# Optimization experiments

Measured on AMD Instinct MI355X. Metric: run time of the kernel, lower is better.

The kernel has to match this reference:

```python
import jax, jax.numpy as jnp
import numpy as np
import math

B, S, D, H = 2, 2048, 1024, 16
DK = D // H  # 64
THETA = 500000.0


def setup_inputs() -> dict:
    key = jax.random.key(0)
    ks = jax.random.split(key, 6)
    x = jax.random.normal(ks[0], (B, S, D), dtype=jnp.float32)
    # RoPE frequencies: inv_freq = theta^{-(2i/dk)}, angles = pos * inv_freq
    inv_freq = 1.0 / (THETA ** (jnp.arange(0, DK, 2, dtype=jnp.float32) / DK))  # [DK/2]
    angles = jnp.arange(S, dtype=jnp.float32)[:, None] * inv_freq[None, :]      # [S, DK/2]
    freqs_cos = jnp.cos(angles)
    freqs_sin = jnp.sin(angles)
    # causal additive mask [B, S, S]: 0 on/below diagonal, -1e9 above
    causal = jnp.tril(jnp.ones((S, S), dtype=bool))
    mask = jnp.where(causal, 0.0, -1e9).astype(jnp.float32)
    mask = jnp.broadcast_to(mask, (B, S, S))
    scale = 0.02
    wq = jax.random.normal(ks[1], (D, D), dtype=jnp.float32) * scale
    wk = jax.random.normal(ks[2], (D, D), dtype=jnp.float32) * scale
    wv = jax.random.normal(ks[3], (D, D), dtype=jnp.float32) * scale
    wo = jax.random.normal(ks[4], (D, D), dtype=jnp.float32) * scale
    return {"x": x, "freqs_cos": freqs_cos, "freqs_sin": freqs_sin,
            "mask": mask, "wq": wq, "wk": wk, "wv": wv, "wo": wo}


def _apply_rope(t, cos, sin):
    # t: [B, S, H, DK]; cos/sin: [S, DK/2]
    tr = t.reshape(*t.shape[:-1], DK // 2, 2)
    t0, t1 = tr[..., 0], tr[..., 1]
    c = cos[None, :, None, :]
    s = sin[None, :, None, :]
    out = jnp.stack([t0 * c - t1 * s, t0 * s + t1 * c], axis=-1)
    return out.reshape(*t.shape)


def reference(x, freqs_cos, freqs_sin, mask, wq, wk, wv, wo):
    b, s, d = x.shape
    # nn.Linear(bias=False): y = x @ W^T, W is [out, in]
    q = jnp.einsum('bsd,ed->bse', x, wq).reshape(b, s, H, DK)
    k = jnp.einsum('bsd,ed->bse', x, wk).reshape(b, s, H, DK)
    v = jnp.einsum('bsd,ed->bse', x, wv).reshape(b, s, H, DK)
    q = _apply_rope(q, freqs_cos, freqs_sin)
    k = _apply_rope(k, freqs_cos, freqs_sin)
    inv_sqrt_dk = 1.0 / math.sqrt(DK)
    # scores: [B, H, S, S]
    scores = jnp.einsum('bqhd,bkhd->bhqk', q, k) * inv_sqrt_dk
    scores = scores + mask[:, None, :, :]
    # NOTE: the original module divides by sqrt(d_k) a SECOND time before softmax
    attn = jax.nn.softmax(scores * inv_sqrt_dk, axis=-1)
    out = jnp.einsum('bhqk,bkhd->bqhd', attn, v).reshape(b, s, d)
    return jnp.einsum('bsd,ed->bse', out, wo)
```

## Files before the change

kernel.cpp:

```cpp
#include <hip/hip_runtime.h>
#include <stdint.h>

#define Bq 2
#define Sq 2048
#define Dq 1024
#define Hq 16
#define DKq 64

typedef unsigned short u16;
typedef __attribute__((ext_vector_type(8))) __bf16 bf8;
typedef __attribute__((ext_vector_type(4))) __bf16 bf4;
typedef __attribute__((ext_vector_type(4))) float fx4;
typedef __attribute__((ext_vector_type(8))) unsigned short us8;
typedef __attribute__((ext_vector_type(4))) unsigned short us4;

__device__ __forceinline__ u16 f2bf(float f) {
    union { float f; unsigned int i; } v; v.f = f;
    unsigned int r = v.i + 0x7FFFu + ((v.i >> 16) & 1u);
    return (u16)(r >> 16);
}

__device__ __forceinline__ void gll16(const void* g, void* l) {
    typedef __attribute__((address_space(1))) void GV;
    typedef __attribute__((address_space(3))) void LV;
    __builtin_amdgcn_global_load_lds((GV*)g, (LV*)l, 16, 0, 0);
}

template<int N> __device__ __forceinline__ void waitv() {
    asm volatile("s_waitcnt vmcnt(%0)" :: "n"(N) : "memory");
}

__global__ void __launch_bounds__(256) cvt_all(const float* __restrict__ x,
                                               const float* __restrict__ wq,
                                               const float* __restrict__ wk,
                                               const float* __restrict__ wv,
                                               const float* __restrict__ wo,
                                               u16* __restrict__ ws) {
    int blk = blockIdx.x;
    const float* s;
    u16* d;
    int i;
    if (blk < 4096)      { s = x;  d = ws;           i = blk * 256 + threadIdx.x; }
    else if (blk < 5120) { s = wq; d = ws + 4194304; i = (blk - 4096) * 256 + threadIdx.x; }
    else if (blk < 6144) { s = wk; d = ws + 5242880; i = (blk - 5120) * 256 + threadIdx.x; }
    else if (blk < 7168) { s = wv; d = ws + 6291456; i = (blk - 6144) * 256 + threadIdx.x; }
    else                 { s = wo; d = ws + 7340032; i = (blk - 7168) * 256 + threadIdx.x; }
    float4 v = *(const float4*)(s + (size_t)i * 4);
    us4 o;
    o[0] = f2bf(v.x); o[1] = f2bf(v.y); o[2] = f2bf(v.z); o[3] = f2bf(v.w);
    *(us4*)(d + (size_t)i * 4) = o;
}

template<int MODE>
__global__ void __launch_bounds__(512, 1) gemm_bt(
    const u16* __restrict__ A,
    const u16* __restrict__ W0, const u16* __restrict__ W1, const u16* __restrict__ W2,
    u16* __restrict__ O0, u16* __restrict__ O1, u16* __restrict__ O2,
    float* __restrict__ Of,
    const float* __restrict__ fc, const float* __restrict__ fs)
{
    constexpr int K = 1024;
    constexpr int NT = 32;
    __shared__ __align__(16) u16 As[3][256 * 32];
    __shared__ __align__(16) u16 Bs[3][256 * 32];
    const int tid = threadIdx.x;
    const int lane = tid & 63, wid = tid >> 6;
    const int wr = wid >> 2, wc = wid & 3;
    const int fr = lane & 15, fq = lane >> 4;

    int wgid = blockIdx.x;
    int Xc = wgid & 7, jj = wgid >> 3;
    int by, bx, bz;
    if (MODE == 1) {
        int T = Xc * 24 + jj;
        by = T / 12;
        int p = T - by * 12;
        bz = p >> 2; bx = p & 3;
    } else {
        int T = Xc * 8 + jj;
        by = T >> 2; bx = T & 3; bz = 0;
    }
    const int m0 = by * 256, n0 = bx * 256;

    const u16* Wm = W0;
    u16* Ob = O0;
    if (MODE == 1) {
        if (bz == 1)      { Wm = W1; Ob = O1; }
        else if (bz == 2) { Wm = W2; Ob = O2; }
    }

    const u16* ga = A  + (size_t)(m0 + (tid >> 2)) * K + (tid & 3) * 8;
    const u16* gb = Wm + (size_t)(n0 + (tid >> 2)) * K + (tid & 3) * 8;

    fx4 acc[8][4] = {};

    auto STAGE_A = [&](int t, int b) {
        gll16(ga + t * 32,           As[b] + tid * 8);
        gll16(ga + 128 * K + t * 32, As[b] + tid * 8 + 4096);
    };
    auto STAGE_B = [&](int t, int b) {
        gll16(gb + t * 32,           Bs[b] + tid * 8);
        gll16(gb + 128 * K + t * 32, Bs[b] + tid * 8 + 4096);
    };

    STAGE_A(0, 0); STAGE_B(0, 0);
    STAGE_A(1, 1); STAGE_B(1, 1);
    waitv<4>();
    __builtin_amdgcn_sched_barrier(0);
    __builtin_amdgcn_s_barrier();
    __builtin_amdgcn_sched_barrier(0);

    int b0 = 0;
    #pragma unroll 1
    for (int t = 0; t < NT; ++t) {
        const u16* Ab = As[b0];
        const u16* Bb = Bs[b0];
        const int bn = b0 + 2 >= 3 ? b0 - 1 : b0 + 2;
        bf8 bfr[4];
        #pragma unroll
        for (int nj = 0; nj < 4; ++nj)
            bfr[nj] = *(const bf8*)(&Bb[(wc * 64 + nj * 16 + fr) * 32 + fq * 8]);

        #pragma unroll
        for (int ph = 0; ph < 2; ++ph) {
            bf8 af[4];
            #pragma unroll
            for (int mi = 0; mi < 4; ++mi)
                af[mi] = *(const bf8*)(&Ab[(wr * 128 + ph * 64 + mi * 16 + fr) * 32 + fq * 8]);
            if (t + 2 < NT) {
                if (ph == 0) STAGE_A(t + 2, bn);
                else         STAGE_B(t + 2, bn);
            }
            __builtin_amdgcn_sched_barrier(0);
            __builtin_amdgcn_s_barrier();
            __builtin_amdgcn_sched_barrier(0);
            __builtin_amdgcn_s_setprio(1);
            #pragma unroll
            for (int mi = 0; mi < 4; ++mi)
                #pragma unroll
                for (int nj = 0; nj < 4; ++nj)
                    acc[ph * 4 + mi][nj] = __builtin_amdgcn_mfma_f32_16x16x32_bf16(
                        af[mi], bfr[nj], acc[ph * 4 + mi][nj], 0, 0, 0);
            __builtin_amdgcn_s_setprio(0);
            __builtin_amdgcn_sched_barrier(0);
            if (ph == 1) {
                if (t < NT - 2) waitv<4>();
                else            waitv<0>();
                __builtin_amdgcn_sched_barrier(0);
            }
            __builtin_amdgcn_s_barrier();
            __builtin_amdgcn_sched_barrier(0);
        }
        b0 = b0 + 1 >= 3 ? 0 : b0 + 1;
    }

    if (MODE == 0) {
        #pragma unroll
        for (int mi = 0; mi < 8; ++mi)
            #pragma unroll
            for (int nj = 0; nj < 4; ++nj)
                #pragma unroll
                for (int r = 0; r < 4; ++r) {
                    int m = m0 + wr * 128 + mi * 16 + fq * 4 + r;
                    int n = n0 + wc * 64 + nj * 16 + fr;
                    Of[(size_t)m * 1024 + n] = acc[mi][nj][r];
                }
    } else if (bz == 2) {
        #pragma unroll
        for (int mi = 0; mi < 8; ++mi)
            #pragma unroll
            for (int nj = 0; nj < 4; ++nj) {
                int n = n0 + wc * 64 + nj * 16 + fr;
                int mb = m0 + wr * 128 + mi * 16 + fq * 4;
                int b = mb >> 11, s = mb & 2047;
                int h = n >> 6, dk = n & 63;
                bf4 pk;
                #pragma unroll
                for (int r = 0; r < 4; ++r) pk[r] = (__bf16)acc[mi][nj][r];
                *(bf4*)((__bf16*)Ob + (((size_t)(b * Hq + h)) * DKq + dk) * Sq + s) = pk;
            }
    } else {
        #pragma unroll
        for (int mi = 0; mi < 8; ++mi)
            #pragma unroll
            for (int nj = 0; nj < 4; ++nj) {
                int n = n0 + wc * 64 + nj * 16 + fr;
                int h = n >> 6, dk = n & 63;
                int ip = dk >> 1;
                float sgn = (dk & 1) ? 1.f : -1.f;
                #pragma unroll
                for (int r = 0; r < 4; ++r) {
                    int m = m0 + wr * 128 + mi * 16 + fq * 4 + r;
                    int b = m >> 11, s = m & 2047;
                    float v = acc[mi][nj][r];
                    float pv = __shfl_xor(v, 1);
                    float c  = fc[s * 32 + ip];
                    float sn = fs[s * 32 + ip];
                    float o = v * c + sgn * pv * sn;
                    ((__bf16*)Ob)[(((size_t)(b * Hq + h)) * Sq + s) * DKq + dk] = (__bf16)o;
                }
            }
    }
}

__device__ __forceinline__ int swz(int row) { return ((row & 7) ^ ((row >> 3) & 7)) << 4; }

__global__ void __launch_bounds__(512, 4) attn_k(const u16* __restrict__ Q,
                                                 const u16* __restrict__ Kg,
                                                 const u16* __restrict__ Vtg,
                                                 u16* __restrict__ AO) {
    int L = blockIdx.x + 32 * blockIdx.y;
    int X = L & 7, C = L >> 3;
    const int bh = X * 4 + (C & 3);
    const int Qt = 31 - (C >> 2);
    const int b = bh >> 4, h = bh & 15;
    const int tid = threadIdx.x, lane = tid & 63, wid = tid >> 6;
    const int wq4 = wid & 3, par = wid >> 2;
    const int fr = lane & 15, fq = lane >> 4;
    const int swzfr = swz(fr);

    __shared__ __align__(16) u16 Ks[2][64 * 64];
    __shared__ __align__(16) u16 Vs[2][64 * 64];
    __shared__ __align__(16) u16 Ps[8][16 * 64];
    __shared__ float Lx[4][64];

    const u16* Kp = Kg  + (size_t)bh * Sq * 64;
    const u16* Vp = Vtg + (size_t)bh * 64 * Sq;
    const int q0 = Qt * 64;
    const int nt = Qt + 1;
    const int NS = (nt + 1) >> 1;

    bf8 qf0, qf1;
    {
        const u16* Qp = Q + ((size_t)bh * Sq + q0) * 64;
        int qr = wq4 * 16 + fr;
        qf0 = *(const bf8*)(Qp + qr * 64 + fq * 8);
        qf1 = *(const bf8*)(Qp + qr * 64 + fq * 8 + 32);
    }

    fx4 oacc[4] = {};
    float l_loc = 0.f;

    const int srow = tid >> 3;
    const int sce  = (tid & 7) * 8;
    const int ldst = srow * 128 + (((tid & 7) * 16) ^ swz(srow));

    us8 kreg[2], vreg[2];
    #pragma unroll
    for (int c = 0; c < 2; ++c) {
        int t = c < nt ? c : nt - 1;
        kreg[c] = *(const us8*)(Kp + ((size_t)t * 64 + srow) * 64 + sce);
        vreg[c] = *(const us8*)(Vp + (size_t)srow * Sq + t * 64 + sce);
    }
    #pragma unroll
    for (int c = 0; c < 2; ++c) {
        *(us8*)((char*)Ks[c] + ldst) = kreg[c];
        *(us8*)((char*)Vs[c] + ldst) = vreg[c];
    }
    if (NS > 1) {
        #pragma unroll
        for (int c = 0; c < 2; ++c) {
            int t = 2 + c < nt ? 2 + c : nt - 1;
            kreg[c] = *(const us8*)(Kp + ((size_t)t * 64 + srow) * 64 + sce);
            vreg[c] = *(const us8*)(Vp + (size_t)srow * Sq + t * 64 + sce);
        }
    }
    __syncthreads();

    #pragma unroll 1
    for (int sp = 0; sp < NS; ++sp) {
        const int t = 2 * sp + par;
        if (t < nt) {
            const char* Kb = (const char*)Ks[par];
            const char* Vb = (const char*)Vs[par];
            char* Pw = (char*)Ps[wid] + fr * 128;

            fx4 sf[4];
            __builtin_amdgcn_s_setprio(1);
            #pragma unroll
            for (int sj = 0; sj < 4; ++sj) {
                int krow = sj * 16 + fr;
                bf8 kf0 = *(const bf8*)(Kb + krow * 128 + ((fq * 16) ^ swz(krow)));
                bf8 kf1 = *(const bf8*)(Kb + krow * 128 + ((64 + fq * 16) ^ swz(krow)));
                fx4 a = {0.f, 0.f, 0.f, 0.f};
                a = __builtin_amdgcn_mfma_f32_16x16x32_bf16(kf0, qf0, a, 0, 0, 0);
                a = __builtin_amdgcn_mfma_f32_16x16x32_bf16(kf1, qf1, a, 0, 0, 0);
                sf[sj] = a;
            }
            __builtin_amdgcn_s_setprio(0);

            float pv[4][4];
            #pragma unroll
            for (int sj = 0; sj < 4; ++sj)
                #pragma unroll
                for (int r = 0; r < 4; ++r)
                    pv[sj][r] = __expf(sf[sj][r] * 0.015625f);
            if (t == Qt) {
                int ql = wq4 * 16 + fr;
                #pragma unroll
                for (int sj = 0; sj < 4; ++sj)
                    #pragma unroll
                    for (int r = 0; r < 4; ++r)
                        if (sj * 16 + fq * 4 + r > ql) pv[sj][r] = 0.f;
            }
            #pragma unroll
            for (int sj = 0; sj < 4; ++sj) {
                bf4 w;
                #pragma unroll
                for (int r = 0; r < 4; ++r) { w[r] = (__bf16)pv[sj][r]; l_loc += pv[sj][r]; }
                *(bf4*)(Pw + ((sj * 32 + fq * 8) ^ swzfr)) = w;
            }

            __builtin_amdgcn_s_setprio(1);
            #pragma unroll
            for (int kk = 0; kk < 2; ++kk) {
                bf8 pf = *(const bf8*)(Pw + ((kk * 64 + fq * 16) ^ swzfr));
                #pragma unroll
                for (int mf = 0; mf < 4; ++mf) {
                    int vrow = mf * 16 + fr;
                    bf8 vf = *(const bf8*)(Vb + vrow * 128 + ((kk * 64 + fq * 16) ^ swz(vrow)));
                    oacc[mf] = __builtin_amdgcn_mfma_f32_16x16x32_bf16(vf, pf, oacc[mf], 0, 0, 0);
                }
            }
            __builtin_amdgcn_s_setprio(0);
        }
        __syncthreads();
        if (sp + 1 < NS) {
            #pragma unroll
            for (int c = 0; c < 2; ++c) {
                *(us8*)((char*)Ks[c] + ldst) = kreg[c];
                *(us8*)((char*)Vs[c] + ldst) = vreg[c];
            }
            if (sp + 2 < NS) {
                #pragma unroll
                for (int c = 0; c < 2; ++c) {
                    int tt = 2 * (sp + 2) + c; if (tt > nt - 1) tt = nt - 1;
                    kreg[c] = *(const us8*)(Kp + ((size_t)tt * 64 + srow) * 64 + sce);
                    vreg[c] = *(const us8*)(Vp + (size_t)srow * Sq + tt * 64 + sce);
                }
            }
            __syncthreads();
        }
    }

    l_loc += __shfl_xor(l_loc, 16);
    l_loc += __shfl_xor(l_loc, 32);
    if (par == 1) {
        float* ob = (float*)Ps + wq4 * 1024;
        #pragma unroll
        for (int mf = 0; mf < 4; ++mf)
            *(fx4*)(ob + lane * 16 + mf * 4) = oacc[mf];
        Lx[wq4][lane] = l_loc;
    }
    __syncthreads();
    if (par == 0) {
        const float* ob = (float*)Ps + wq4 * 1024;
        float lt = l_loc + Lx[wq4][lane];
        float linv = __builtin_amdgcn_rcpf(lt);
        int s = q0 + wq4 * 16 + fr;
        #pragma unroll
        for (int mf = 0; mf < 4; ++mf) {
            fx4 oh = *(const fx4*)(ob + lane * 16 + mf * 4);
            bf4 pk;
            #pragma unroll
            for (int r = 0; r < 4; ++r) pk[r] = (__bf16)((oacc[mf][r] + oh[r]) * linv);
            *(bf4*)((__bf16*)AO + ((size_t)(b * Sq + s)) * Dq + h * 64 + mf * 16 + fq * 4) = pk;
        }
    }
}

extern "C" void kernel_launch(void* const* d_in, const int* in_sizes, int n_in,
                              void* d_out, int out_size, void* d_ws, size_t ws_size,
                              hipStream_t stream) {
    const float* x  = (const float*)d_in[0];
    const float* fc = (const float*)d_in[1];
    const float* fs = (const float*)d_in[2];
    const float* wq = (const float*)d_in[4];
    const float* wk = (const float*)d_in[5];
    const float* wv = (const float*)d_in[6];
    const float* wo = (const float*)d_in[7];
    float* out = (float*)d_out;

    u16* ws  = (u16*)d_ws;
    u16* xb  = ws;
    u16* wqb = ws + 4194304;
    u16* wkb = ws + 5242880;
    u16* wvb = ws + 6291456;
    u16* wob = ws + 7340032;
    u16* Qb  = ws + 8388608;
    u16* Kb  = ws + 12582912;
    u16* Vb  = ws + 16777216;
    u16* AOb = ws + 20971520;

    cvt_all<<<8192, 256, 0, stream>>>(x, wq, wk, wv, wo, ws);

    gemm_bt<1><<<192, 512, 0, stream>>>(xb, wqb, wkb, wvb, Qb, Kb, Vb, nullptr, fc, fs);

    dim3 g2(32, 32, 1);
    attn_k<<<g2, 512, 0, stream>>>(Qb, Kb, Vb, AOb);

    gemm_bt<0><<<64, 512, 0, stream>>>(AOb, wob, nullptr, nullptr, nullptr, nullptr, nullptr, out, nullptr, nullptr);
}
```

Measured before the change: 128.1 us.

## Shrink GEMM tiles to 128-row blocks, add LDS swizzle and deeper prefetch

The projection GEMMs move from 256x256 tiles to 128x256 (QKV) and 128x128 (output) tiles, raising block counts from 192/64 to 384/256 so more of the GPU's compute units are filled. Launch bounds now allow up to 4 blocks per SM. An XOR swizzle on the K-column chunk is added to cut LDS bank conflicts, and the pipeline is simplified to one phase per k-step with three stages prefetched up front. The trade-off is less data reuse per tile and more global traffic per FLOP.

```diff
diff --git a/kernel.cpp b/kernel.cpp
--- a/kernel.cpp
+++ b/kernel.cpp
@@ -29,6 +29,7 @@
 template<int N> __device__ __forceinline__ void waitv() {
     asm volatile("s_waitcnt vmcnt(%0)" :: "n"(N) : "memory");
 }
+__device__ __forceinline__ void SB() { __builtin_amdgcn_sched_barrier(0); }
 
 __global__ void __launch_bounds__(256) cvt_all(const float* __restrict__ x,
                                                const float* __restrict__ wq,
@@ -52,7 +53,7 @@
 }
 
 template<int MODE>
-__global__ void __launch_bounds__(512, 1) gemm_bt(
+__global__ void __launch_bounds__(512, 4) gemm_bt(
     const u16* __restrict__ A,
     const u16* __restrict__ W0, const u16* __restrict__ W1, const u16* __restrict__ W2,
     u16* __restrict__ O0, u16* __restrict__ O1, u16* __restrict__ O2,
@@ -61,8 +62,15 @@
 {
     constexpr int K = 1024;
     constexpr int NT = 32;
-    __shared__ __align__(16) u16 As[3][256 * 32];
-    __shared__ __align__(16) u16 Bs[3][256 * 32];
+    constexpr int BN = MODE ? 256 : 128;
+    constexpr int WN = BN / 4;
+    constexpr int NJ = WN / 16;
+    constexpr int BOPS = BN / 128;
+    constexpr int SOPS = 1 + BOPS;
+    constexpr int ASZ = 128 * 32;
+    constexpr int BSZ = BN * 32;
+    __shared__ __align__(16) u16 As[3 * ASZ];
+    __shared__ __align__(16) u16 Bs[3 * BSZ];
     const int tid = threadIdx.x;
     const int lane = tid & 63, wid = tid >> 6;
     const int wr = wid >> 2, wc = wid & 3;
@@ -72,15 +80,15 @@
     int Xc = wgid & 7, jj = wgid >> 3;
     int by, bx, bz;
     if (MODE == 1) {
-        int T = Xc * 24 + jj;
+        int T = Xc * 48 + jj;
         by = T / 12;
         int p = T - by * 12;
         bz = p >> 2; bx = p & 3;
     } else {
-        int T = Xc * 8 + jj;
-        by = T >> 2; bx = T & 3; bz = 0;
-    }
-    const int m0 = by * 256, n0 = bx * 256;
+        int T = Xc * 32 + jj;
+        by = T >> 3; bx = T & 7; bz = 0;
+    }
+    const int m0 = by * 128, n0 = bx * BN;
 
     const u16* Wm = W0;
     u16* Ob = O0;
@@ -89,89 +97,69 @@
         else if (bz == 2) { Wm = W2; Ob = O2; }
     }
 
-    const u16* ga = A  + (size_t)(m0 + (tid >> 2)) * K + (tid & 3) * 8;
-    const u16* gb = Wm + (size_t)(n0 + (tid >> 2)) * K + (tid & 3) * 8;
-
-    fx4 acc[8][4] = {};
-
-    auto STAGE_A = [&](int t, int b) {
-        gll16(ga + t * 32,           As[b] + tid * 8);
-        gll16(ga + 128 * K + t * 32, As[b] + tid * 8 + 4096);
+    const int arow = tid >> 2;
+    const int scol = (((tid & 3) ^ (arow & 3)) * 8);
+    const u16* ga = A  + (size_t)(m0 + arow) * K + scol;
+    const u16* gb = Wm + (size_t)(n0 + arow) * K + scol;
+
+    fx4 acc[4][NJ] = {};
+
+    auto STAGE = [&](int t, int b) {
+        gll16(ga + t * 32, As + b * ASZ + tid * 8);
+        #pragma unroll
+        for (int c = 0; c < BOPS; ++c)
+            gll16(gb + (size_t)c * 128 * K + t * 32, Bs + b * BSZ + c * 4096 + tid * 8);
     };
-    auto STAGE_B = [&](int t, int b) {
-        gll16(gb + t * 32,           Bs[b] + tid * 8);
-        gll16(gb + 128 * K + t * 32, Bs[b] + tid * 8 + 4096);
-    };
-
-    STAGE_A(0, 0); STAGE_B(0, 0);
-    STAGE_A(1, 1); STAGE_B(1, 1);
-    waitv<4>();
-    __builtin_amdgcn_sched_barrier(0);
-    __builtin_amdgcn_s_barrier();
-    __builtin_amdgcn_sched_barrier(0);
-
-    int b0 = 0;
+
+    const int kq = (fq ^ (fr & 3)) * 8;
+
+    STAGE(0, 0); STAGE(1, 1); STAGE(2, 2);
+    waitv<2 * SOPS>();
+    SB(); __builtin_amdgcn_s_barrier(); SB();
+
     #pragma unroll 1
     for (int t = 0; t < NT; ++t) {
-        const u16* Ab = As[b0];
-        const u16* Bb = Bs[b0];
-        const int bn = b0 + 2 >= 3 ? b0 - 1 : b0 + 2;
-        bf8 bfr[4];
-        #pragma unroll
-        for (int nj = 0; nj < 4; ++nj)
-            bfr[nj] = *(const bf8*)(&Bb[(wc * 64 + nj * 16 + fr) * 32 + fq * 8]);
-
-        #pragma unroll
-        for (int ph = 0; ph < 2; ++ph) {
-            bf8 af[4];
-            #pragma unroll
-            for (int mi = 0; mi < 4; ++mi)
-                af[mi] = *(const bf8*)(&Ab[(wr * 128 + ph * 64 + mi * 16 + fr) * 32 + fq * 8]);
-            if (t + 2 < NT) {
-                if (ph == 0) STAGE_A(t + 2, bn);
-                else         STAGE_B(t + 2, bn);
-            }
-            __builtin_amdgcn_sched_barrier(0);
-            __builtin_amdgcn_s_barrier();
-            __builtin_amdgcn_sched_barrier(0);
-            __builtin_amdgcn_s_setprio(1);
-            #pragma unroll
-            for (int mi = 0; mi < 4; ++mi)
-                #pragma unroll
-                for (int nj = 0; nj < 4; ++nj)
-                    acc[ph * 4 + mi][nj] = __builtin_amdgcn_mfma_f32_16x16x32_bf16(
-                        af[mi], bfr[nj], acc[ph * 4 + mi][nj], 0, 0, 0);
-            __builtin_amdgcn_s_setprio(0);
-            __builtin_amdgcn_sched_barrier(0);
-            if (ph == 1) {
-                if (t < NT - 2) waitv<4>();
-                else            waitv<0>();
-                __builtin_amdgcn_sched_barrier(0);
-            }
-            __builtin_amdgcn_s_barrier();
-            __builtin_amdgcn_sched_barrier(0);
-        }
-        b0 = b0 + 1 >= 3 ? 0 : b0 + 1;
+        const u16* Ab = As + (t % 3) * ASZ;
+        const u16* Bb = Bs + (t % 3) * BSZ;
+        bf8 af[4], bf[NJ];
+        #pragma unroll
+        for (int mi = 0; mi < 4; ++mi)
+            af[mi] = *(const bf8*)(&Ab[(wr * 64 + mi * 16 + fr) * 32 + kq]);
+        #pragma unroll
+        for (int nj = 0; nj < NJ; ++nj)
+            bf[nj] = *(const bf8*)(&Bb[(wc * WN + nj * 16 + fr) * 32 + kq]);
+        if (t + 2 < NT) STAGE(t + 2, (t + 2) % 3);
+        __builtin_amdgcn_s_setprio(1);
+        #pragma unroll
+        for (int mi = 0; mi < 4; ++mi)
+            #pragma unroll
+            for (int nj = 0; nj < NJ; ++nj)
+                acc[mi][nj] = __builtin_amdgcn_mfma_f32_16x16x32_bf16(af[mi], bf[nj], acc[mi][nj], 0, 0, 0);
+        __builtin_amdgcn_s_setprio(0);
+        SB();
+        if (t < NT - 2)       { waitv<SOPS>(); }
+        else if (t == NT - 2) { waitv<0>(); }
+        SB(); __builtin_amdgcn_s_barrier(); SB();
     }
 
     if (MODE == 0) {
         #pragma unroll
-        for (int mi = 0; mi < 8; ++mi)
-            #pragma unroll
-            for (int nj = 0; nj < 4; ++nj)
+        for (int mi = 0; mi < 4; ++mi)
+            #pragma unroll
+            for (int nj = 0; nj < NJ; ++nj)
                 #pragma unroll
                 for (int r = 0; r < 4; ++r) {
-                    int m = m0 + wr * 128 + mi * 16 + fq * 4 + r;
-                    int n = n0 + wc * 64 + nj * 16 + fr;
+                    int m = m0 + wr * 64 + mi * 16 + fq * 4 + r;
+                    int n = n0 + wc * WN + nj * 16 + fr;
                     Of[(size_t)m * 1024 + n] = acc[mi][nj][r];
                 }
     } else if (bz == 2) {
         #pragma unroll
-        for (int mi = 0; mi < 8; ++mi)
-            #pragma unroll
-            for (int nj = 0; nj < 4; ++nj) {
-                int n = n0 + wc * 64 + nj * 16 + fr;
-                int mb = m0 + wr * 128 + mi * 16 + fq * 4;
+        for (int mi = 0; mi < 4; ++mi)
+            #pragma unroll
+            for (int nj = 0; nj < NJ; ++nj) {
+                int n = n0 + wc * WN + nj * 16 + fr;
+                int mb = m0 + wr * 64 + mi * 16 + fq * 4;
                 int b = mb >> 11, s = mb & 2047;
                 int h = n >> 6, dk = n & 63;
                 bf4 pk;
@@ -181,16 +169,16 @@
             }
     } else {
         #pragma unroll
-        for (int mi = 0; mi < 8; ++mi)
-            #pragma unroll
-            for (int nj = 0; nj < 4; ++nj) {
-                int n = n0 + wc * 64 + nj * 16 + fr;
+        for (int mi = 0; mi < 4; ++mi)
+            #pragma unroll
+            for (int nj = 0; nj < NJ; ++nj) {
+                int n = n0 + wc * WN + nj * 16 + fr;
                 int h = n >> 6, dk = n & 63;
                 int ip = dk >> 1;
                 float sgn = (dk & 1) ? 1.f : -1.f;
                 #pragma unroll
                 for (int r = 0; r < 4; ++r) {
-                    int m = m0 + wr * 128 + mi * 16 + fq * 4 + r;
+                    int m = m0 + wr * 64 + mi * 16 + fq * 4 + r;
                     int b = m >> 11, s = m & 2047;
                     float v = acc[mi][nj][r];
                     float pv = __shfl_xor(v, 1);
@@ -394,10 +382,10 @@
 
     cvt_all<<<8192, 256, 0, stream>>>(x, wq, wk, wv, wo, ws);
 
-    gemm_bt<1><<<192, 512, 0, stream>>>(xb, wqb, wkb, wvb, Qb, Kb, Vb, nullptr, fc, fs);
+    gemm_bt<1><<<384, 512, 0, stream>>>(xb, wqb, wkb, wvb, Qb, Kb, Vb, nullptr, fc, fs);
 
     dim3 g2(32, 32, 1);
     attn_k<<<g2, 512, 0, stream>>>(Qb, Kb, Vb, AOb);
 
-    gemm_bt<0><<<64, 512, 0, stream>>>(AOb, wob, nullptr, nullptr, nullptr, nullptr, nullptr, out, nullptr, nullptr);
-}
+    gemm_bt<0><<<256, 512, 0, stream>>>(AOb, wob, nullptr, nullptr, nullptr, nullptr, nullptr, out, nullptr, nullptr);
+}
```

Measured after the change: 104.7 us. -18.3%, faster.
